# Kernel optimization log

Measured on AMD Instinct MI355X. Metric: run time of the kernel, lower is better.

## Reference

```python
import jax, jax.numpy as jnp
import numpy as np

# Dims: V = in-simplices, E = out-simplices, K = input_ch, C = target_ch,
#       D = in_depth_ch, O = o_depth_ch
V = 8192
E = 8192
K = 64
C = 64
D = 8
O = 8


def setup_inputs() -> dict:
    key = jax.random.key(0)
    k1, k2, k3, k4 = jax.random.split(key, 4)
    x = jax.random.normal(k1, (V, K, D), dtype=jnp.float32)
    G = jax.random.normal(k2, (E, V), dtype=jnp.float32) * 0.02  # dense boundary operator
    # o_depth_ch stacked TensorLinear weights: W[o, d, k, c], bias b[o, c, d]
    W = jax.random.normal(k3, (O, D, K, C), dtype=jnp.float32) * (1.0 / np.sqrt(K))
    b = jax.random.normal(k4, (O, C, D), dtype=jnp.float32) * 0.02
    return {"x": x, "G": G, "W": W, "b": b}


def reference(x, G, W, b):
    # Per out-depth channel o: y_o[v,c,d] = sum_k x[v,k,d] * W[o,d,k,c] + b[o,c,d]
    # output[e,c,o] = sum_{v,d} G[e,v] * y_o[v,c,d]
    # Fuse: sum over d inside the first contraction; bias contributes
    # rowsum(G)[e] * sum_d b[o,c,d].
    z = jnp.einsum('vkd,odkc->ovc', x, W) + b.sum(axis=-1)[:, None, :]  # [O, V, C]
    out = jnp.einsum('ev,ovc->eco', G, z)                               # [E, C, O]
    return out
```

## Files before the change

kernel.cpp:

```cpp
#include <hip/hip_runtime.h>
#include <hip/hip_bf16.h>

#define V_DIM 8192
#define E_DIM 8192
#define KD    512
#define CO    512

typedef __attribute__((ext_vector_type(8))) short short8;
typedef __attribute__((ext_vector_type(8))) unsigned short ushort8;
typedef __attribute__((ext_vector_type(4))) float f32x4;

__device__ __forceinline__ unsigned short f2b(float f) {
  __hip_bfloat16 h = __float2bfloat16(f);
  return __builtin_bit_cast(unsigned short, h);
}

__device__ __forceinline__ void gload_lds16(const void* g, void* l) {
  __builtin_amdgcn_global_load_lds(
      (const __attribute__((address_space(1))) void*)g,
      (__attribute__((address_space(3))) void*)l, 16, 0, 0);
}

__global__ void convert_x(const float* __restrict__ x, unsigned short* __restrict__ xb) {
  const size_t i = ((size_t)blockIdx.x * 256 + threadIdx.x) * 8;
  float4 f0 = *(const float4*)(x + i);
  float4 f1 = *(const float4*)(x + i + 4);
  ushort8 u;
  u[0]=f2b(f0.x); u[1]=f2b(f0.y); u[2]=f2b(f0.z); u[3]=f2b(f0.w);
  u[4]=f2b(f1.x); u[5]=f2b(f1.y); u[6]=f2b(f1.z); u[7]=f2b(f1.w);
  *(ushort8*)(xb + i) = u;
}

__global__ void repack_w(const float* __restrict__ W, const float* __restrict__ b,
                         float* __restrict__ Wt, float* __restrict__ bsum) {
  const int idx = blockIdx.x * 256 + threadIdx.x;
  const int j = idx >> 9, kd = idx & 511;
  const int c = j >> 3, o = j & 7, k = kd >> 3, d = kd & 7;
  Wt[idx] = W[(((o * 8 + d) * 64 + k) << 6) + c];
  if (idx < 512) {
    const int cc = idx >> 3, oo = idx & 7;
    float s = 0.f;
#pragma unroll
    for (int dd = 0; dd < 8; ++dd) s += b[((oo * 64 + cc) << 3) + dd];
    bsum[idx] = s;
  }
}

template<int NT, bool OUT_BF16, bool HASBIAS, bool SWIZ>
__global__ __launch_bounds__(512, 2)
void gemm_bt(const float* __restrict__ A, const unsigned short* __restrict__ B,
             const float* __restrict__ bias, void* __restrict__ Cout,
             int ldA, int ldB, int ldC) {
  static_assert((NT - 2) % 6 == 0, "pipeline needs (NT-2) divisible by 6");
  __shared__ __align__(16) unsigned short As[3][128 * 64];
  __shared__ __align__(16) unsigned short Bs[3][128 * 64];

  const int tid  = threadIdx.x;
  const int lane = tid & 63;
  const int w    = tid >> 6;
  const int wm   = w >> 2;
  const int wn   = w & 3;

  int bm, bn;
  if (SWIZ) {
    int bid = blockIdx.x + (blockIdx.y << 2);
    bid = ((bid & 7) << 5) | (bid >> 3);
    bm = bid >> 2; bn = bid & 3;
  } else {
    bm = blockIdx.y; bn = blockIdx.x;
  }
  const int m0 = bm * 128, n0 = bn * 128;

  const int sr  = tid >> 3;
  const int sc  = tid & 7;
  const int brl = lane >> 3;
  const int bch = lane & 7;

  const float* agB0 = A + (size_t)(m0 + sr) * ldA + sc * 8;
  const float* agB1 = agB0 + (size_t)64 * ldA;
  const int aw0 = sr * 64 + ((sc ^ (sr & 7)) * 8);
  const int aw1 = aw0 + 64 * 64;

  const unsigned short* bsrc0 =
      B + (size_t)(n0 + w * 8 + brl) * ldB + ((bch ^ brl) * 8);
  const unsigned short* bsrc1 = bsrc0 + (size_t)64 * ldB;
  const int bd0 = (w * 8) * 64;
  const int bd1 = (64 + w * 8) * 64;

  f32x4 acc[4][2];
#pragma unroll
  for (int i = 0; i < 4; ++i)
#pragma unroll
    for (int j = 0; j < 2; ++j) acc[i][j] = (f32x4)0.0f;

  f32x4 pf[2][4];

#define STAGE_LOAD(T, C, SLOT) do {                                       \
    const int kt_ = (T) << 6;                                             \
    pf[(C)][0] = *(const f32x4*)(agB0 + kt_);                             \
    pf[(C)][1] = *(const f32x4*)(agB0 + kt_ + 4);                         \
    pf[(C)][2] = *(const f32x4*)(agB1 + kt_);                             \
    pf[(C)][3] = *(const f32x4*)(agB1 + kt_ + 4);                         \
    gload_lds16(bsrc0 + kt_, &Bs[(SLOT)][bd0]);                           \
    gload_lds16(bsrc1 + kt_, &Bs[(SLOT)][bd1]);                           \
  } while (0)

#define STAGE_WRITE(C, SLOT) do {                                         \
    ushort8 u0_, u1_;                                                     \
    u0_[0]=f2b(pf[(C)][0][0]); u0_[1]=f2b(pf[(C)][0][1]);                 \
    u0_[2]=f2b(pf[(C)][0][2]); u0_[3]=f2b(pf[(C)][0][3]);                 \
    u0_[4]=f2b(pf[(C)][1][0]); u0_[5]=f2b(pf[(C)][1][1]);                 \
    u0_[6]=f2b(pf[(C)][1][2]); u0_[7]=f2b(pf[(C)][1][3]);                 \
    u1_[0]=f2b(pf[(C)][2][0]); u1_[1]=f2b(pf[(C)][2][1]);                 \
    u1_[2]=f2b(pf[(C)][2][2]); u1_[3]=f2b(pf[(C)][2][3]);                 \
    u1_[4]=f2b(pf[(C)][3][0]); u1_[5]=f2b(pf[(C)][3][1]);                 \
    u1_[6]=f2b(pf[(C)][3][2]); u1_[7]=f2b(pf[(C)][3][3]);                 \
    *(ushort8*)(&As[(SLOT)][aw0]) = u0_;                                  \
    *(ushort8*)(&As[(SLOT)][aw1]) = u1_;                                  \
  } while (0)

#define COMPUTE(SLOT) do {                                                \
    const unsigned short* Ab_ = As[(SLOT)];                               \
    const unsigned short* Bb_ = Bs[(SLOT)];                               \
    _Pragma("unroll")                                                     \
    for (int kk = 0; kk < 2; ++kk) {                                      \
      const int ck_ = kk * 4 + (lane >> 4);                               \
      short8 af_[4], bf_[2];                                              \
      _Pragma("unroll")                                                   \
      for (int mi = 0; mi < 4; ++mi) {                                    \
        const int r_ = wm * 64 + mi * 16 + (lane & 15);                   \
        af_[mi] = *(const short8*)(Ab_ + r_ * 64 + ((ck_ ^ (r_ & 7)) * 8)); \
      }                                                                   \
      _Pragma("unroll")                                                   \
      for (int ni = 0; ni < 2; ++ni) {                                    \
        const int r_ = wn * 32 + ni * 16 + (lane & 15);                   \
        bf_[ni] = *(const short8*)(Bb_ + r_ * 64 + ((ck_ ^ (r_ & 7)) * 8)); \
      }                                                                   \
      _Pragma("unroll")                                                   \
      for (int mi = 0; mi < 4; ++mi)                                      \
        _Pragma("unroll")                                                 \
        for (int ni = 0; ni < 2; ++ni)                                    \
          acc[mi][ni] = __builtin_amdgcn_mfma_f32_16x16x32_bf16(          \
              af_[mi], bf_[ni], acc[mi][ni], 0, 0, 0);                    \
    }                                                                     \
  } while (0)

  STAGE_LOAD(0, 0, 0);
  STAGE_LOAD(1, 1, 1);
  STAGE_WRITE(0, 0);

#pragma unroll 1
  for (int tb = 0; tb < NT - 2; tb += 6) {
#pragma unroll
    for (int jj = 0; jj < 6; ++jj) {
      STAGE_LOAD(tb + jj + 2, jj & 1, (jj + 2) % 3);
      asm volatile("s_waitcnt vmcnt(6)" ::: "memory");
      STAGE_WRITE((jj + 1) & 1, (jj + 1) % 3);
      asm volatile("s_waitcnt lgkmcnt(0)" ::: "memory");
      __builtin_amdgcn_sched_barrier(0);
      __builtin_amdgcn_s_barrier();
      __builtin_amdgcn_sched_barrier(0);
      COMPUTE(jj % 3);
      __builtin_amdgcn_sched_barrier(0);
      __builtin_amdgcn_s_barrier();
    }
  }

  asm volatile("s_waitcnt vmcnt(0)" ::: "memory");
  STAGE_WRITE((NT - 1) & 1, (NT - 1) % 3);
  asm volatile("s_waitcnt lgkmcnt(0)" ::: "memory");
  __builtin_amdgcn_sched_barrier(0);
  __builtin_amdgcn_s_barrier();
  __builtin_amdgcn_sched_barrier(0);
  COMPUTE((NT - 2) % 3);
  __builtin_amdgcn_sched_barrier(0);
  __builtin_amdgcn_s_barrier();
  COMPUTE((NT - 1) % 3);

#undef STAGE_LOAD
#undef STAGE_WRITE
#undef COMPUTE

  const int rg = lane >> 4;
  const int cl = lane & 15;
#pragma unroll
  for (int mi = 0; mi < 4; ++mi) {
#pragma unroll
    for (int r = 0; r < 4; ++r) {
      const int row = m0 + wm * 64 + mi * 16 + rg * 4 + r;
      float bv = 0.0f;
      if (HASBIAS) bv = bias[row];
#pragma unroll
      for (int ni = 0; ni < 2; ++ni) {
        const int col = n0 + wn * 32 + ni * 16 + cl;
        const float v = acc[mi][ni][r] + bv;
        if (OUT_BF16)
          ((unsigned short*)Cout)[(size_t)row * ldC + col] = f2b(v);
        else
          ((float*)Cout)[(size_t)row * ldC + col] = v;
      }
    }
  }
}

extern "C" void kernel_launch(void* const* d_in, const int* in_sizes, int n_in,
                              void* d_out, int out_size, void* d_ws, size_t ws_size,
                              hipStream_t stream) {
  const float* x = (const float*)d_in[0];
  const float* G = (const float*)d_in[1];
  const float* W = (const float*)d_in[2];
  const float* b = (const float*)d_in[3];

  char* ws = (char*)d_ws;
  unsigned short* xb = (unsigned short*)ws;
  float* Wt          = (float*)(ws + (8u << 20));
  float* bs          = (float*)(ws + (9u << 20));
  unsigned short* Zt = (unsigned short*)(ws + (9u << 20) + (1u << 16));

  hipLaunchKernelGGL(convert_x, dim3(2048), dim3(256), 0, stream, x, xb);
  hipLaunchKernelGGL(repack_w, dim3(1024), dim3(256), 0, stream, W, b, Wt, bs);

  hipLaunchKernelGGL((gemm_bt<8, true, true, false>), dim3(64, 4), dim3(512), 0,
                     stream, Wt, xb, bs, (void*)Zt, KD, KD, V_DIM);

  hipLaunchKernelGGL((gemm_bt<128, false, false, true>), dim3(4, 64), dim3(512), 0,
                     stream, G, Zt, (const float*)nullptr, (void*)d_out,
                     V_DIM, V_DIM, CO);
}
```

Baseline: 502.9 us.

## Reorder GEMM pipeline to compute before A-tile write and shrink A LDS buffers

Restructures the software pipeline in the bt GEMM. Each iteration now issues global loads, computes on the current tile, and only then converts and writes the next A tile to LDS. This lets the global-load latency overlap with the MFMA work instead of waiting before compute. The A shared buffer drops from three slots to two, while B keeps three because its global_load_lds writes land asynchronously. The barrier count per iteration stays the same, and the smaller LDS footprint may allow better occupancy.

```diff
diff --git a/kernel.cpp b/kernel.cpp
--- a/kernel.cpp
+++ b/kernel.cpp
@@ -52,7 +52,7 @@
              const float* __restrict__ bias, void* __restrict__ Cout,
              int ldA, int ldB, int ldC) {
   static_assert((NT - 2) % 6 == 0, "pipeline needs (NT-2) divisible by 6");
-  __shared__ __align__(16) unsigned short As[3][128 * 64];
+  __shared__ __align__(16) unsigned short As[2][128 * 64];
   __shared__ __align__(16) unsigned short Bs[3][128 * 64];
 
   const int tid  = threadIdx.x;
@@ -95,17 +95,17 @@
 
   f32x4 pf[2][4];
 
-#define STAGE_LOAD(T, C, SLOT) do {                                       \
+#define STAGE_LOAD(T, C, BSLOT) do {                                      \
     const int kt_ = (T) << 6;                                             \
     pf[(C)][0] = *(const f32x4*)(agB0 + kt_);                             \
     pf[(C)][1] = *(const f32x4*)(agB0 + kt_ + 4);                         \
     pf[(C)][2] = *(const f32x4*)(agB1 + kt_);                             \
     pf[(C)][3] = *(const f32x4*)(agB1 + kt_ + 4);                         \
-    gload_lds16(bsrc0 + kt_, &Bs[(SLOT)][bd0]);                           \
-    gload_lds16(bsrc1 + kt_, &Bs[(SLOT)][bd1]);                           \
-  } while (0)
-
-#define STAGE_WRITE(C, SLOT) do {                                         \
+    gload_lds16(bsrc0 + kt_, &Bs[(BSLOT)][bd0]);                          \
+    gload_lds16(bsrc1 + kt_, &Bs[(BSLOT)][bd1]);                          \
+  } while (0)
+
+#define STAGE_WRITE(C, ASLOT) do {                                        \
     ushort8 u0_, u1_;                                                     \
     u0_[0]=f2b(pf[(C)][0][0]); u0_[1]=f2b(pf[(C)][0][1]);                 \
     u0_[2]=f2b(pf[(C)][0][2]); u0_[3]=f2b(pf[(C)][0][3]);                 \
@@ -115,13 +115,13 @@
     u1_[2]=f2b(pf[(C)][2][2]); u1_[3]=f2b(pf[(C)][2][3]);                 \
     u1_[4]=f2b(pf[(C)][3][0]); u1_[5]=f2b(pf[(C)][3][1]);                 \
     u1_[6]=f2b(pf[(C)][3][2]); u1_[7]=f2b(pf[(C)][3][3]);                 \
-    *(ushort8*)(&As[(SLOT)][aw0]) = u0_;                                  \
-    *(ushort8*)(&As[(SLOT)][aw1]) = u1_;                                  \
-  } while (0)
-
-#define COMPUTE(SLOT) do {                                                \
-    const unsigned short* Ab_ = As[(SLOT)];                               \
-    const unsigned short* Bb_ = Bs[(SLOT)];                               \
+    *(ushort8*)(&As[(ASLOT)][aw0]) = u0_;                                 \
+    *(ushort8*)(&As[(ASLOT)][aw1]) = u1_;                                 \
+  } while (0)
+
+#define COMPUTE(ASLOT, BSLOT) do {                                        \
+    const unsigned short* Ab_ = As[(ASLOT)];                              \
+    const unsigned short* Bb_ = Bs[(BSLOT)];                              \
     _Pragma("unroll")                                                     \
     for (int kk = 0; kk < 2; ++kk) {                                      \
       const int ck_ = kk * 4 + (lane >> 4);                               \
@@ -145,41 +145,45 @@
     }                                                                     \
   } while (0)
 
+#define BAR() do {                                                        \
+    __builtin_amdgcn_sched_barrier(0);                                    \
+    __builtin_amdgcn_s_barrier();                                         \
+    __builtin_amdgcn_sched_barrier(0);                                    \
+  } while (0)
+
   STAGE_LOAD(0, 0, 0);
   STAGE_LOAD(1, 1, 1);
+  asm volatile("s_waitcnt vmcnt(6)" ::: "memory");
   STAGE_WRITE(0, 0);
+  asm volatile("s_waitcnt lgkmcnt(0)" ::: "memory");
+  BAR();
 
 #pragma unroll 1
   for (int tb = 0; tb < NT - 2; tb += 6) {
 #pragma unroll
     for (int jj = 0; jj < 6; ++jj) {
       STAGE_LOAD(tb + jj + 2, jj & 1, (jj + 2) % 3);
+      COMPUTE(jj & 1, jj % 3);
+      BAR();
       asm volatile("s_waitcnt vmcnt(6)" ::: "memory");
-      STAGE_WRITE((jj + 1) & 1, (jj + 1) % 3);
+      STAGE_WRITE((jj + 1) & 1, (jj + 1) & 1);
       asm volatile("s_waitcnt lgkmcnt(0)" ::: "memory");
-      __builtin_amdgcn_sched_barrier(0);
-      __builtin_amdgcn_s_barrier();
-      __builtin_amdgcn_sched_barrier(0);
-      COMPUTE(jj % 3);
-      __builtin_amdgcn_sched_barrier(0);
-      __builtin_amdgcn_s_barrier();
+      BAR();
     }
   }
 
+  COMPUTE((NT - 2) & 1, (NT - 2) % 3);
+  BAR();
   asm volatile("s_waitcnt vmcnt(0)" ::: "memory");
-  STAGE_WRITE((NT - 1) & 1, (NT - 1) % 3);
+  STAGE_WRITE((NT - 1) & 1, (NT - 1) & 1);
   asm volatile("s_waitcnt lgkmcnt(0)" ::: "memory");
-  __builtin_amdgcn_sched_barrier(0);
-  __builtin_amdgcn_s_barrier();
-  __builtin_amdgcn_sched_barrier(0);
-  COMPUTE((NT - 2) % 3);
-  __builtin_amdgcn_sched_barrier(0);
-  __builtin_amdgcn_s_barrier();
-  COMPUTE((NT - 1) % 3);
+  BAR();
+  COMPUTE((NT - 1) & 1, (NT - 1) % 3);
 
 #undef STAGE_LOAD
 #undef STAGE_WRITE
 #undef COMPUTE
+#undef BAR
 
   const int rg = lane >> 4;
   const int cl = lane & 15;
```

After: 474.7 us. 5.6% less time.
